# Kernel tuning notes

Hardware: AMD Instinct MI355X
Metric: run time of the kernel (lower is better)

The kernel has to match this reference:

```python
import jax, jax.numpy as jnp
import numpy as np
import math

B, L, D, H, MAX_K = 8, 4096, 2048, 16, 1024
HD = D // H


def setup_inputs() -> dict:
    key = jax.random.key(0)
    ks = jax.random.split(key, 20)
    x = jax.random.normal(ks[0], (B, L, D), dtype=jnp.float32)
    register = jax.random.normal(ks[1], (B, D), dtype=jnp.float32)
    # mask with exactly MAX_K True per row -> max_k == MAX_K, no ragged padding
    perms = jax.vmap(lambda k: jax.random.permutation(k, L))(jax.random.split(ks[2], B))
    sel = perms[:, :MAX_K]
    mask = jnp.zeros((B, L), dtype=bool).at[jnp.arange(B)[:, None], sel].set(True)
    s = 1.0 / math.sqrt(D)
    def lin(k):
        k1, k2 = jax.random.split(k)
        return (jax.random.uniform(k1, (D, D), jnp.float32, -s, s),
                jax.random.uniform(k2, (D,), jnp.float32, -s, s))
    Wq, bq = lin(ks[3]); Wk, bk = lin(ks[4]); Wv, bv = lin(ks[5])
    Wrk, brk = lin(ks[6]); Wrv, brv = lin(ks[7]); Wo, bo = lin(ks[8])
    return {"x": x, "mask": mask, "register": register,
            "Wq": Wq, "bq": bq, "Wk": Wk, "bk": bk, "Wv": Wv, "bv": bv,
            "Wrk": Wrk, "brk": brk, "Wrv": Wrv, "brv": brv, "Wo": Wo, "bo": bo}


def reference(x, mask, register, Wq, bq, Wk, bk, Wv, bv, Wrk, brk, Wrv, brv, Wo, bo):
    Bb, Ll, Dd = x.shape
    scale = math.sqrt(HD)
    # stable argsort puts True(=selected) tokens first, in ascending position order
    idx = jnp.argsort(jnp.logical_not(mask), axis=1, stable=True)[:, :MAX_K]  # [B,K]
    pos = idx
    sig = jnp.take_along_axis(x, idx[:, :, None], axis=1)  # [B,K,D]
    Q = (sig @ Wq.T + bq).reshape(Bb, MAX_K, H, HD)
    Kt = (sig @ Wk.T + bk)
    Vt = (sig @ Wv.T + bv)
    Kr = (register @ Wrk.T + brk)[:, None, :]  # [B,1,D]
    Vr = (register @ Wrv.T + brv)[:, None, :]
    Kall = jnp.concatenate([Kt, Kr], axis=1).reshape(Bb, MAX_K + 1, H, HD)
    Vall = jnp.concatenate([Vt, Vr], axis=1).reshape(Bb, MAX_K + 1, H, HD)
    scores = jnp.einsum('bqhd,bkhd->bhqk', Q, Kall) / scale  # [B,H,K,K+1]
    causal = jnp.where(pos[:, :, None] < pos[:, None, :], -1e9, 0.0)  # [B,K,K]
    full_mask = jnp.concatenate([causal, jnp.zeros((Bb, MAX_K, 1), x.dtype)], axis=2)[:, None]
    attn = jax.nn.softmax(scores + full_mask, axis=-1)
    out = jnp.einsum('bhqk,bkhd->bqhd', attn, Vall).reshape(Bb, MAX_K, Dd)
    y = out @ Wo.T + bo
    res = x.at[jnp.arange(Bb)[:, None], idx].set(y)
    return res
```

## Files before the change

### kernel.cpp

```cpp
#include <hip/hip_runtime.h>
#include <hip/hip_bf16.h>

#define B_  8
#define L_  4096
#define D_  2048
#define H_  16
#define HD_ 128
#define MK_ 1024
#define VTP 1040

typedef __attribute__((ext_vector_type(8))) short short8;
typedef __attribute__((ext_vector_type(4))) float f32x4;

__device__ inline unsigned short f2bf(float f) {
  unsigned int u = __float_as_uint(f);
  unsigned int r = (u + 0x7fffu + ((u >> 16) & 1u)) >> 16;
  return (unsigned short)r;
}

__device__ __forceinline__ void gload_lds16(const void* g, void* l) {
  __builtin_amdgcn_global_load_lds(
      (const __attribute__((address_space(1))) void*)g,
      (__attribute__((address_space(3))) void*)l, 16, 0, 0);
}

__global__ void detect_mask_kernel(const unsigned char* __restrict__ mask, int* flag,
                                   unsigned char* __restrict__ sel) {
  __shared__ int cnt;
  if (threadIdx.x == 0) cnt = 0;
  __syncthreads();
  for (int i = threadIdx.x; i < (B_ * L_) / 16; i += 256) ((int4*)sel)[i] = make_int4(0, 0, 0, 0);
  int local = 0;
  for (int i = threadIdx.x; i < B_ * L_; i += 256) local += (mask[i] != 0);
  atomicAdd(&cnt, local);
  __syncthreads();
  if (threadIdx.x == 0) {
    int t = 0;
    if (cnt == B_ * MK_)      t = 0;
    else if (cnt == 2 * MK_)  t = 1;
    else if (cnt == 4 * MK_)  t = 2;
    *flag = t;
  }
}

__global__ void build_rowmap_kernel(const void* __restrict__ maskv,
                                    const int* __restrict__ flag,
                                    int* __restrict__ rowmap,
                                    unsigned char* __restrict__ sel) {
  int b = blockIdx.x;
  int tid = threadIdx.x;
  int t = *flag;
  __shared__ int cnts[256];
  unsigned char loc[16];
  int c = 0;
  for (int j = 0; j < 16; ++j) {
    int pos = tid * 16 + j;
    int mv;
    if (t == 1)      mv = ((const int*)maskv)[b * L_ + pos] != 0;
    else if (t == 2) mv = ((const float*)maskv)[b * L_ + pos] != 0.0f;
    else             mv = ((const unsigned char*)maskv)[b * L_ + pos] != 0;
    loc[j] = (unsigned char)mv; c += mv;
  }
  cnts[tid] = c;
  __syncthreads();
  for (int off = 1; off < 256; off <<= 1) {
    int v = (tid >= off) ? cnts[tid - off] : 0;
    __syncthreads();
    cnts[tid] += v;
    __syncthreads();
  }
  int rank = cnts[tid] - c;
  for (int j = 0; j < 16; ++j) {
    if (loc[j]) {
      if (rank < MK_) {
        int grow = b * L_ + tid * 16 + j;
        rowmap[b * MK_ + rank] = grow;
        sel[grow] = 1;
      }
      ++rank;
    }
  }
}

__global__ __launch_bounds__(256) void copy_x_kernel(const float4* __restrict__ src,
                                                     float4* __restrict__ dst,
                                                     const unsigned char* __restrict__ sel) {
  int row = blockIdx.x;
  if (sel[row]) return;
  size_t base = (size_t)row * 512 + threadIdx.x;
  dst[base] = src[base];
  dst[base + 256] = src[base + 256];
}

__global__ __launch_bounds__(256) void gather_sig_kernel(const float* __restrict__ x,
                                                         const int* __restrict__ rowmap,
                                                         unsigned short* __restrict__ sig) {
  int row = blockIdx.x;
  const float* src = x + (size_t)rowmap[row] * D_;
  unsigned short* dst = sig + (size_t)row * D_;
  int tid = threadIdx.x;
  float4 a = ((const float4*)src)[tid * 2];
  float4 b4 = ((const float4*)src)[tid * 2 + 1];
  uint4 o;
  o.x = f2bf(a.x)  | ((unsigned)f2bf(a.y)  << 16);
  o.y = f2bf(a.z)  | ((unsigned)f2bf(a.w)  << 16);
  o.z = f2bf(b4.x) | ((unsigned)f2bf(b4.y) << 16);
  o.w = f2bf(b4.z) | ((unsigned)f2bf(b4.w) << 16);
  *(uint4*)(dst + tid * 8) = o;
}

__global__ __launch_bounds__(256) void conv_bf16_kernel(const float* __restrict__ W,
                                                        unsigned short* __restrict__ Wb) {
  size_t i = ((size_t)blockIdx.x * 256 + threadIdx.x) * 8;
  float4 a = *(const float4*)(W + i);
  float4 b4 = *(const float4*)(W + i + 4);
  uint4 o;
  o.x = f2bf(a.x)  | ((unsigned)f2bf(a.y)  << 16);
  o.y = f2bf(a.z)  | ((unsigned)f2bf(a.w)  << 16);
  o.z = f2bf(b4.x) | ((unsigned)f2bf(b4.y) << 16);
  o.w = f2bf(b4.z) | ((unsigned)f2bf(b4.w) << 16);
  *(uint4*)(Wb + i) = o;
}

__global__ __launch_bounds__(256) void reg_kv_kernel(
    const float* __restrict__ reg, const float* __restrict__ Wrk, const float* __restrict__ brk,
    const float* __restrict__ Wrv, const float* __restrict__ brv,
    unsigned short* __restrict__ Kb, unsigned short* __restrict__ Vt) {
  int gw = (blockIdx.x * 256 + threadIdx.x) >> 6;
  int lane = threadIdx.x & 63;
  int mat = gw >> 11;
  int n = gw & 2047;
  const float* W = mat ? Wrv : Wrk;
  const float* wrow = W + (size_t)n * D_;
  float s[8] = {};
  for (int j = 0; j < 8; ++j) {
    int e = j * 256 + lane * 4;
    float4 wv = *(const float4*)(wrow + e);
#pragma unroll
    for (int b = 0; b < 8; ++b) {
      float4 rv = *(const float4*)(reg + (size_t)b * D_ + e);
      s[b] += wv.x * rv.x + wv.y * rv.y + wv.z * rv.z + wv.w * rv.w;
    }
  }
#pragma unroll
  for (int off = 32; off; off >>= 1)
#pragma unroll
    for (int b = 0; b < 8; ++b) s[b] += __shfl_down(s[b], off);
  if (lane == 0) {
    float bias = (mat ? brv : brk)[n];
#pragma unroll
    for (int b = 0; b < 8; ++b) {
      unsigned short v = f2bf(s[b] + bias);
      if (mat) {
        Vt[(((size_t)b * 16 + (n >> 7)) * 128 + (n & 127)) * VTP + 1024] = v;
      } else {
        Kb[((size_t)b * 1025 + 1024) * D_ + n] = v;
      }
    }
  }
}

template<int OUT_MODE>
__global__ __launch_bounds__(512, 2) void gemm8_kernel(
    const unsigned short* __restrict__ A, const unsigned short* __restrict__ Bw,
    const float* __restrict__ bias, void* __restrict__ Cout,
    const int* __restrict__ rowmap, float alpha) {
  __shared__ __align__(16) unsigned short lds[4][2][8192];
  int tid = threadIdx.x, lane = tid & 63, w = tid >> 6;
  int g = lane >> 4, l15 = lane & 15;
  int wm = w >> 2, wn = w & 3;

  int bid = blockIdx.x;
  int xcd = bid & 7, j = bid >> 3;
  int mb = xcd * 4 + (j >> 3), nb = j & 7;
  int m0 = mb * 256, n0 = nb * 256;

  f32x4 acc[2][4][4] = {};

#define STAGE(kt, c) {                                                          \
    const unsigned short* src0 = (c) ? Bw : A;                                  \
    int base0 = (c) ? n0 : m0;                                                  \
    int sg = (lane & 3) ^ ((lane >> 3) & 3);                                    \
    _Pragma("unroll")                                                           \
    for (int i_ = 0; i_ < 2; ++i_) {                                            \
      int row = (w * 2 + i_) * 16 + (lane >> 2);                                \
      gload_lds16(src0 + (size_t)(base0 + row) * D_ + (kt) * 32 + sg * 8,       \
                  &lds[(kt) & 3][c][(w * 2 + i_) * 512]);                       \
    }                                                                           \
  }

  STAGE(0, 0); STAGE(0, 1);
  STAGE(1, 0); STAGE(1, 1);
  asm volatile("s_waitcnt vmcnt(4)" ::: "memory");
  __builtin_amdgcn_s_barrier();

  int sw8 = (g ^ ((l15 >> 1) & 3)) * 8;

  for (int kt = 0; kt < 64; ++kt) {
    const unsigned short* Abuf = &lds[kt & 3][0][0];
    const unsigned short* Bbuf = &lds[kt & 3][1][0];
    short8 af[4], bf[4];

#pragma unroll
    for (int nf = 0; nf < 4; ++nf)
      bf[nf] = *(const short8*)(Bbuf + (wn * 64 + nf * 16 + l15) * 32 + sw8);
#pragma unroll
    for (int mf = 0; mf < 4; ++mf)
      af[mf] = *(const short8*)(Abuf + (wm * 128 + mf * 16 + l15) * 32 + sw8);
    if (kt + 2 < 64) STAGE(kt + 2, 0);
    __builtin_amdgcn_s_barrier();
    asm volatile("s_waitcnt lgkmcnt(0)" ::: "memory");
    __builtin_amdgcn_sched_barrier(0);
    __builtin_amdgcn_s_setprio(1);
#pragma unroll
    for (int mf = 0; mf < 4; ++mf)
#pragma unroll
      for (int nf = 0; nf < 4; ++nf)
        acc[0][mf][nf] = __builtin_amdgcn_mfma_f32_16x16x32_bf16(af[mf], bf[nf], acc[0][mf][nf], 0, 0, 0);
    __builtin_amdgcn_s_setprio(0);
    __builtin_amdgcn_s_barrier();

#pragma unroll
    for (int mf = 0; mf < 4; ++mf)
      af[mf] = *(const short8*)(Abuf + (wm * 128 + 64 + mf * 16 + l15) * 32 + sw8);
    if (kt + 2 < 64) STAGE(kt + 2, 1);
    __builtin_amdgcn_s_barrier();
    asm volatile("s_waitcnt lgkmcnt(0)" ::: "memory");
    __builtin_amdgcn_sched_barrier(0);
    __builtin_amdgcn_s_setprio(1);
#pragma unroll
    for (int mf = 0; mf < 4; ++mf)
#pragma unroll
      for (int nf = 0; nf < 4; ++nf)
        acc[1][mf][nf] = __builtin_amdgcn_mfma_f32_16x16x32_bf16(af[mf], bf[nf], acc[1][mf][nf], 0, 0, 0);
    __builtin_amdgcn_s_setprio(0);
    if (kt < 62)       asm volatile("s_waitcnt vmcnt(4)" ::: "memory");
    else if (kt == 62) asm volatile("s_waitcnt vmcnt(0)" ::: "memory");
    __builtin_amdgcn_s_barrier();
  }
#undef STAGE

#pragma unroll
  for (int ph = 0; ph < 2; ++ph) {
#pragma unroll
    for (int mf = 0; mf < 4; ++mf) {
#pragma unroll
      for (int nf = 0; nf < 4; ++nf) {
        int nn = n0 + wn * 64 + nf * 16 + l15;
        float bvv = bias[nn];
        int m = m0 + wm * 128 + ph * 64 + mf * 16 + g * 4;
        if (OUT_MODE == 3) {
          int bb = m >> 10, tok = m & 1023;
          size_t base = (((size_t)bb * 16 + (nn >> 7)) * 128 + (nn & 127)) * VTP + tok;
          uint2 u;
          u.x = f2bf(acc[ph][mf][nf][0] + bvv) | ((unsigned)f2bf(acc[ph][mf][nf][1] + bvv) << 16);
          u.y = f2bf(acc[ph][mf][nf][2] + bvv) | ((unsigned)f2bf(acc[ph][mf][nf][3] + bvv) << 16);
          *(uint2*)((unsigned short*)Cout + base) = u;
        } else {
#pragma unroll
          for (int r = 0; r < 4; ++r) {
            float v = (acc[ph][mf][nf][r] + bvv) * alpha;
            if (OUT_MODE == 0) {
              ((unsigned short*)Cout)[(size_t)(m + r) * D_ + nn] = f2bf(v);
            } else if (OUT_MODE == 1) {
              int row = (m + r) + ((m + r) >> 10);
              ((unsigned short*)Cout)[(size_t)row * D_ + nn] = f2bf(v);
            } else {
              int row = rowmap[m + r];
              ((float*)Cout)[(size_t)row * D_ + nn] = v;
            }
          }
        }
      }
    }
  }
}

__device__ __forceinline__ void stage_k(const unsigned short* Kbase, unsigned short* dst,
                                        int kv0, int w, int lane) {
#pragma unroll
  for (int i = 0; i < 2; ++i) {
    int ib = w * 2 + i;
    int row = ib * 4 + (lane >> 4);
    int sl = (lane & 15) ^ (row & 7);
    int krow = kv0 + row; if (krow > MK_) krow = MK_;
    gload_lds16(Kbase + (size_t)krow * D_ + sl * 8, dst + ib * 512);
  }
}
__device__ __forceinline__ void stage_v(const unsigned short* Vbase, unsigned short* dst,
                                        int kv0, int w, int lane) {
#pragma unroll
  for (int i = 0; i < 2; ++i) {
    int ib = w * 2 + i;
    int row = ib * 8 + (lane >> 3);
    int sl = (lane & 7) ^ (row & 7);
    gload_lds16(Vbase + (size_t)row * VTP + kv0 + sl * 8, dst + ib * 512);
  }
}

__global__ __launch_bounds__(512) void attn_kernel(
    const unsigned short* __restrict__ Qb, const unsigned short* __restrict__ Kb,
    const unsigned short* __restrict__ Vt, unsigned short* __restrict__ Ob) {
  int bx = blockIdx.x;
  int qi = 7 - (bx >> 7);
  int bh = bx & 127;
  int b = bh >> 4, h = bh & 15;
  int tid = threadIdx.x, lane = tid & 63, w = tid >> 6;
  int g = lane >> 4, l15 = lane & 15;
  int q0 = qi * 128;
  int nt = 2 * qi + 3;

  __shared__ __align__(16) unsigned short Ks[2][64 * 128];
  __shared__ __align__(16) unsigned short Vts[128 * 64];
  __shared__ __align__(16) unsigned short Ps[8][16][72];

  const unsigned short* Kbase = Kb + (size_t)b * 1025 * D_ + h * HD_;
  const unsigned short* Vbase = Vt + (size_t)bh * 128 * VTP;

  short8 qf[4];
  {
    const unsigned short* qrow = Qb + (size_t)(b * MK_ + q0 + w * 16 + l15) * D_ + h * HD_;
#pragma unroll
    for (int kk = 0; kk < 4; ++kk) qf[kk] = *(const short8*)(qrow + kk * 32 + g * 8);
  }

  f32x4 oacc[8] = {};
  float mrow[4], lrow[4];
#pragma unroll
  for (int r = 0; r < 4; ++r) { mrow[r] = -__builtin_inff(); lrow[r] = 0.f; }

  int qminw = q0 + w * 16;

  stage_k(Kbase, Ks[0], 0, w, lane);
  int cur = 0;

  for (int t = 0; t < nt; ++t) {
    int kv0 = (t < nt - 1) ? t * 64 : MK_;
    stage_v(Vbase, Vts, kv0, w, lane);
    if (t + 1 < nt) {
      int kv1 = (t + 1 < nt - 1) ? (t + 1) * 64 : MK_;
      stage_k(Kbase, Ks[cur ^ 1], kv1, w, lane);
      asm volatile("s_waitcnt vmcnt(4)" ::: "memory");
    } else {
      asm volatile("s_waitcnt vmcnt(2)" ::: "memory");
    }
    __builtin_amdgcn_s_barrier();

    bool active = (t == nt - 1) || (t * 64 <= qminw + 15);
    f32x4 sacc[4] = {};
    if (active) {
      const unsigned short* ks = Ks[cur];
#pragma unroll
      for (int kk = 0; kk < 4; ++kk) {
#pragma unroll
        for (int nf = 0; nf < 4; ++nf) {
          int krow = nf * 16 + l15;
          int sw = (kk * 4 + g) ^ (krow & 7);
          short8 kf = *(const short8*)(ks + krow * 128 + sw * 8);
          sacc[nf] = __builtin_amdgcn_mfma_f32_16x16x32_bf16(qf[kk], kf, sacc[nf], 0, 0, 0);
        }
      }

      if (t == nt - 1) {
#pragma unroll
        for (int nf = 0; nf < 4; ++nf) {
          int col = nf * 16 + l15;
          if (col != 0) {
#pragma unroll
            for (int r = 0; r < 4; ++r) sacc[nf][r] = -1e9f;
          }
        }
      } else if (t * 64 + 63 > qminw) {
        int qb = qminw - t * 64 + g * 4;
#pragma unroll
        for (int nf = 0; nf < 4; ++nf) {
          int col = nf * 16 + l15;
#pragma unroll
          for (int r = 0; r < 4; ++r)
            if (col > qb + r) sacc[nf][r] = -1e9f;
        }
      }

      float pm[4]; bool need = false;
#pragma unroll
      for (int r = 0; r < 4; ++r) {
        float mx = fmaxf(fmaxf(sacc[0][r], sacc[1][r]), fmaxf(sacc[2][r], sacc[3][r]));
        mx = fmaxf(mx, __shfl_xor(mx, 1));
        mx = fmaxf(mx, __shfl_xor(mx, 2));
        mx = fmaxf(mx, __shfl_xor(mx, 4));
        mx = fmaxf(mx, __shfl_xor(mx, 8));
        pm[r] = mx;
        need |= (mx > mrow[r] + 8.0f);
      }
      if (__any((int)need)) {
#pragma unroll
        for (int r = 0; r < 4; ++r) {
          float mnew = fmaxf(mrow[r], pm[r]);
          float sf = exp2f(mrow[r] - mnew);
          mrow[r] = mnew;
          lrow[r] *= sf;
#pragma unroll
          for (int i = 0; i < 8; ++i) oacc[i][r] *= sf;
        }
      }
      float rs[4] = {0.f, 0.f, 0.f, 0.f};
#pragma unroll
      for (int nf = 0; nf < 4; ++nf) {
#pragma unroll
        for (int r = 0; r < 4; ++r) {
          float p = exp2f(sacc[nf][r] - mrow[r]);
          sacc[nf][r] = p;
          rs[r] += p;
        }
      }
#pragma unroll
      for (int r = 0; r < 4; ++r) {
        float s = rs[r];
        s += __shfl_xor(s, 1);
        s += __shfl_xor(s, 2);
        s += __shfl_xor(s, 4);
        s += __shfl_xor(s, 8);
        lrow[r] += s;
      }
#pragma unroll
      for (int nf = 0; nf < 4; ++nf)
#pragma unroll
        for (int r = 0; r < 4; ++r)
          Ps[w][g * 4 + r][nf * 16 + l15] = f2bf(sacc[nf][r]);
    }

    if (t + 1 < nt) asm volatile("s_waitcnt vmcnt(2)" ::: "memory");
    else            asm volatile("s_waitcnt vmcnt(0)" ::: "memory");
    __builtin_amdgcn_s_barrier();

    if (active) {
#pragma unroll
      for (int kk = 0; kk < 2; ++kk) {
        short8 pf = *(const short8*)(&Ps[w][l15][kk * 32 + g * 8]);
#pragma unroll
        for (int nf = 0; nf < 8; ++nf) {
          int vrow = nf * 16 + l15;
          int sw = (kk * 4 + g) ^ (vrow & 7);
          short8 vf = *(const short8*)(Vts + vrow * 64 + sw * 8);
          oacc[nf] = __builtin_amdgcn_mfma_f32_16x16x32_bf16(pf, vf, oacc[nf], 0, 0, 0);
        }
      }
    }
    __builtin_amdgcn_s_barrier();
    cur ^= 1;
  }

#pragma unroll
  for (int nf = 0; nf < 8; ++nf) {
#pragma unroll
    for (int r = 0; r < 4; ++r) {
      size_t row = (size_t)b * MK_ + q0 + w * 16 + g * 4 + r;
      Ob[row * D_ + h * HD_ + nf * 16 + l15] = f2bf(oacc[nf][r] / lrow[r]);
    }
  }
}

extern "C" void kernel_launch(void* const* d_in, const int* in_sizes, int n_in,
                              void* d_out, int out_size, void* d_ws, size_t ws_size,
                              hipStream_t stream) {
  const float* x    = (const float*)d_in[0];
  const void*  mask = d_in[1];
  const float* reg  = (const float*)d_in[2];
  const float* Wq   = (const float*)d_in[3];
  const float* bq   = (const float*)d_in[4];
  const float* Wk   = (const float*)d_in[5];
  const float* bk   = (const float*)d_in[6];
  const float* Wv   = (const float*)d_in[7];
  const float* bv   = (const float*)d_in[8];
  const float* Wrk  = (const float*)d_in[9];
  const float* brk  = (const float*)d_in[10];
  const float* Wrv  = (const float*)d_in[11];
  const float* brv  = (const float*)d_in[12];
  const float* Wo   = (const float*)d_in[13];
  const float* bo   = (const float*)d_in[14];

  char* ws = (char*)d_ws;
  int* flag            = (int*)ws;
  int* rowmap          = (int*)(ws + 256);
  unsigned char* sel   = (unsigned char*)(ws + 33024);
  char* p = ws + 66048;
  unsigned short* sig = (unsigned short*)p;              p += (size_t)8192 * 2048 * 2;
  unsigned short* Qb  = (unsigned short*)p;              p += (size_t)8192 * 2048 * 2;
  unsigned short* Kb  = (unsigned short*)p;              p += (size_t)8200 * 2048 * 2;
  unsigned short* Vtb = (unsigned short*)p;              p += ((size_t)16384 * VTP + 64) * 2;
  unsigned short* Wbf = (unsigned short*)p;              p += (size_t)2048 * 2048 * 2;
  unsigned short* Ob  = sig;

  detect_mask_kernel<<<1, 256, 0, stream>>>((const unsigned char*)mask, flag, sel);
  build_rowmap_kernel<<<8, 256, 0, stream>>>(mask, flag, rowmap, sel);
  copy_x_kernel<<<B_ * L_, 256, 0, stream>>>((const float4*)x, (float4*)d_out, sel);
  gather_sig_kernel<<<8192, 256, 0, stream>>>(x, rowmap, sig);
  reg_kv_kernel<<<1024, 256, 0, stream>>>(reg, Wrk, brk, Wrv, brv, Kb, Vtb);

  const float qalpha = 0.08838834764831845f * 1.4426950408889634f;
  conv_bf16_kernel<<<2048, 256, 0, stream>>>(Wq, Wbf);
  gemm8_kernel<0><<<256, 512, 0, stream>>>(sig, Wbf, bq, Qb, nullptr, qalpha);
  conv_bf16_kernel<<<2048, 256, 0, stream>>>(Wk, Wbf);
  gemm8_kernel<1><<<256, 512, 0, stream>>>(sig, Wbf, bk, Kb, nullptr, 1.0f);
  conv_bf16_kernel<<<2048, 256, 0, stream>>>(Wv, Wbf);
  gemm8_kernel<3><<<256, 512, 0, stream>>>(sig, Wbf, bv, Vtb, nullptr, 1.0f);
  attn_kernel<<<1024, 512, 0, stream>>>(Qb, Kb, Vtb, Ob);
  conv_bf16_kernel<<<2048, 256, 0, stream>>>(Wo, Wbf);
  gemm8_kernel<2><<<256, 512, 0, stream>>>(Ob, Wbf, bo, d_out, rowmap, 1.0f);
}
```

Before: 549.8 us.

## Fuse Q, K and V projections into a single wide GEMM launch

New measurement: 554.6 us. Within noise of the previous version (+0.9%).

```diff
diff --git a/kernel.cpp b/kernel.cpp
--- a/kernel.cpp
+++ b/kernel.cpp
@@ -160,11 +160,12 @@
   }
 }
 
-template<int OUT_MODE>
+template<int FUSED>
 __global__ __launch_bounds__(512, 2) void gemm8_kernel(
     const unsigned short* __restrict__ A, const unsigned short* __restrict__ Bw,
-    const float* __restrict__ bias, void* __restrict__ Cout,
-    const int* __restrict__ rowmap, float alpha) {
+    const float* __restrict__ b0, const float* __restrict__ b1, const float* __restrict__ b2,
+    void* __restrict__ O0, void* __restrict__ O1, void* __restrict__ O2,
+    const int* __restrict__ rowmap, float qalpha, int nbt, int matfix) {
   __shared__ __align__(16) unsigned short lds[4][2][8192];
   int tid = threadIdx.x, lane = tid & 63, w = tid >> 6;
   int g = lane >> 4, l15 = lane & 15;
@@ -172,7 +173,7 @@
 
   int bid = blockIdx.x;
   int xcd = bid & 7, j = bid >> 3;
-  int mb = xcd * 4 + (j >> 3), nb = j & 7;
+  int mb = xcd * 4 + j / nbt, nb = j % nbt;
   int m0 = mb * 256, n0 = nb * 256;
 
   f32x4 acc[2][4][4] = {};
@@ -240,35 +241,49 @@
   }
 #undef STAGE
 
+  int mat = 0;
+  const float* bias = b0;
+  float alpha = 1.0f;
+  int n0l = n0;
+  if (FUSED) {
+    mat = (matfix >= 0) ? matfix : (n0 >> 11);
+    bias = (mat == 0) ? b0 : ((mat == 1) ? b1 : b2);
+    alpha = (mat == 0) ? qalpha : 1.0f;
+    n0l = n0 & 2047;
+  }
+
 #pragma unroll
   for (int ph = 0; ph < 2; ++ph) {
 #pragma unroll
     for (int mf = 0; mf < 4; ++mf) {
 #pragma unroll
       for (int nf = 0; nf < 4; ++nf) {
-        int nn = n0 + wn * 64 + nf * 16 + l15;
+        int nn = n0l + wn * 64 + nf * 16 + l15;
         float bvv = bias[nn];
         int m = m0 + wm * 128 + ph * 64 + mf * 16 + g * 4;
-        if (OUT_MODE == 3) {
-          int bb = m >> 10, tok = m & 1023;
-          size_t base = (((size_t)bb * 16 + (nn >> 7)) * 128 + (nn & 127)) * VTP + tok;
-          uint2 u;
-          u.x = f2bf(acc[ph][mf][nf][0] + bvv) | ((unsigned)f2bf(acc[ph][mf][nf][1] + bvv) << 16);
-          u.y = f2bf(acc[ph][mf][nf][2] + bvv) | ((unsigned)f2bf(acc[ph][mf][nf][3] + bvv) << 16);
-          *(uint2*)((unsigned short*)Cout + base) = u;
+        if (FUSED) {
+          if (mat == 2) {
+            int bb = m >> 10, tok = m & 1023;
+            size_t base = (((size_t)bb * 16 + (nn >> 7)) * 128 + (nn & 127)) * VTP + tok;
+            uint2 u;
+            u.x = f2bf(acc[ph][mf][nf][0] + bvv) | ((unsigned)f2bf(acc[ph][mf][nf][1] + bvv) << 16);
+            u.y = f2bf(acc[ph][mf][nf][2] + bvv) | ((unsigned)f2bf(acc[ph][mf][nf][3] + bvv) << 16);
+            *(uint2*)((unsigned short*)O2 + base) = u;
+          } else {
+            unsigned short* out = (mat == 0) ? (unsigned short*)O0 : (unsigned short*)O1;
+#pragma unroll
+            for (int r = 0; r < 4; ++r) {
+              float v = (acc[ph][mf][nf][r] + bvv) * alpha;
+              int mm = m + r;
+              int row = (mat == 1) ? mm + (mm >> 10) : mm;
+              out[(size_t)row * D_ + nn] = f2bf(v);
+            }
+          }
         } else {
 #pragma unroll
           for (int r = 0; r < 4; ++r) {
-            float v = (acc[ph][mf][nf][r] + bvv) * alpha;
-            if (OUT_MODE == 0) {
-              ((unsigned short*)Cout)[(size_t)(m + r) * D_ + nn] = f2bf(v);
-            } else if (OUT_MODE == 1) {
-              int row = (m + r) + ((m + r) >> 10);
-              ((unsigned short*)Cout)[(size_t)row * D_ + nn] = f2bf(v);
-            } else {
-              int row = rowmap[m + r];
-              ((float*)Cout)[(size_t)row * D_ + nn] = v;
-            }
+            int row = rowmap[m + r];
+            ((float*)O0)[(size_t)row * D_ + nn] = acc[ph][mf][nf][r] + bvv;
           }
         }
       }
@@ -488,8 +503,11 @@
   unsigned short* Qb  = (unsigned short*)p;              p += (size_t)8192 * 2048 * 2;
   unsigned short* Kb  = (unsigned short*)p;              p += (size_t)8200 * 2048 * 2;
   unsigned short* Vtb = (unsigned short*)p;              p += ((size_t)16384 * VTP + 64) * 2;
-  unsigned short* Wbf = (unsigned short*)p;              p += (size_t)2048 * 2048 * 2;
+  unsigned short* Wbf = (unsigned short*)p;
   unsigned short* Ob  = sig;
+
+  const size_t need_fused = (size_t)(p - ws) + (size_t)6144 * 2048 * 2;
+  const bool fused = (ws_size >= need_fused);
 
   detect_mask_kernel<<<1, 256, 0, stream>>>((const unsigned char*)mask, flag, sel);
   build_rowmap_kernel<<<8, 256, 0, stream>>>(mask, flag, rowmap, sel);
@@ -498,13 +516,26 @@
   reg_kv_kernel<<<1024, 256, 0, stream>>>(reg, Wrk, brk, Wrv, brv, Kb, Vtb);
 
   const float qalpha = 0.08838834764831845f * 1.4426950408889634f;
-  conv_bf16_kernel<<<2048, 256, 0, stream>>>(Wq, Wbf);
-  gemm8_kernel<0><<<256, 512, 0, stream>>>(sig, Wbf, bq, Qb, nullptr, qalpha);
-  conv_bf16_kernel<<<2048, 256, 0, stream>>>(Wk, Wbf);
-  gemm8_kernel<1><<<256, 512, 0, stream>>>(sig, Wbf, bk, Kb, nullptr, 1.0f);
-  conv_bf16_kernel<<<2048, 256, 0, stream>>>(Wv, Wbf);
-  gemm8_kernel<3><<<256, 512, 0, stream>>>(sig, Wbf, bv, Vtb, nullptr, 1.0f);
+
+  if (fused) {
+    conv_bf16_kernel<<<2048, 256, 0, stream>>>(Wq, Wbf);
+    conv_bf16_kernel<<<2048, 256, 0, stream>>>(Wk, Wbf + (size_t)2048 * 2048);
+    conv_bf16_kernel<<<2048, 256, 0, stream>>>(Wv, Wbf + (size_t)4096 * 2048);
+    gemm8_kernel<1><<<768, 512, 0, stream>>>(sig, Wbf, bq, bk, bv, Qb, Kb, Vtb,
+                                             nullptr, qalpha, 24, -1);
+  } else {
+    conv_bf16_kernel<<<2048, 256, 0, stream>>>(Wq, Wbf);
+    gemm8_kernel<1><<<256, 512, 0, stream>>>(sig, Wbf, bq, bk, bv, Qb, Kb, Vtb,
+                                             nullptr, qalpha, 8, 0);
+    conv_bf16_kernel<<<2048, 256, 0, stream>>>(Wk, Wbf);
+    gemm8_kernel<1><<<256, 512, 0, stream>>>(sig, Wbf, bq, bk, bv, Qb, Kb, Vtb,
+                                             nullptr, qalpha, 8, 1);
+    conv_bf16_kernel<<<2048, 256, 0, stream>>>(Wv, Wbf);
+    gemm8_kernel<1><<<256, 512, 0, stream>>>(sig, Wbf, bq, bk, bv, Qb, Kb, Vtb,
+                                             nullptr, qalpha, 8, 2);
+  }
   attn_kernel<<<1024, 512, 0, stream>>>(Qb, Kb, Vtb, Ob);
   conv_bf16_kernel<<<2048, 256, 0, stream>>>(Wo, Wbf);
-  gemm8_kernel<2><<<256, 512, 0, stream>>>(Ob, Wbf, bo, d_out, rowmap, 1.0f);
-}
+  gemm8_kernel<0><<<256, 512, 0, stream>>>(Ob, Wbf, bo, nullptr, nullptr, d_out, nullptr, nullptr,
+                                           rowmap, 1.0f, 8, -1);
+}
```
